# Performance work log

Hardware: AMD Instinct MI355X
Metric: run time of the kernel (lower is better)

## Reference

```python
import jax, jax.numpy as jnp
import numpy as np

DIM_Z = 32      # latent Kalman state dim
DIM_Y = 16      # pseudo-observation dim
K_CLUST = 64    # number of switching clusters
T = 128         # sequence_length
BATCH = 256     # batch_size
INIT_COV = 20.0
NOISE_Q = 0.08  # noise_transition
NOISE_R = 0.03  # noise_emission
INIT_KF = 0.05  # init_kf_matrices (C init scale)


def setup_inputs() -> dict:
    key = jax.random.key(0)
    k1, k2, k3, k4, k5 = jax.random.split(key, 5)
    y = jax.random.normal(k1, (BATCH, T, DIM_Y), jnp.float32)
    dist = jax.random.normal(k2, (BATCH, T, K_CLUST), jnp.float32)
    # A initialized as identity per cluster (plus tiny perturbation so grads are non-trivial)
    A = jnp.broadcast_to(jnp.eye(DIM_Z, dtype=jnp.float32), (K_CLUST, DIM_Z, DIM_Z)) \
        + 0.01 * jax.random.normal(k3, (K_CLUST, DIM_Z, DIM_Z), jnp.float32)
    Bm = 0.01 * jax.random.normal(k4, (K_CLUST, DIM_Z), jnp.float32)  # bias (zeros-init in original)
    C = INIT_KF * jax.random.normal(k5, (K_CLUST, DIM_Y, DIM_Z), jnp.float32)
    return {"y": y, "dist": dist, "A": A, "Bm": Bm, "C": C}


def reference(y, dist, A, Bm, C):
    Q = NOISE_Q * jnp.eye(DIM_Z, dtype=y.dtype)
    R = NOISE_R * jnp.eye(DIM_Y, dtype=y.dtype)
    I = jnp.eye(DIM_Z, dtype=y.dtype)

    mu0 = jnp.zeros((BATCH, DIM_Z), y.dtype)
    Sigma0 = INIT_COV * jnp.broadcast_to(jnp.eye(DIM_Z, dtype=y.dtype), (BATCH, DIM_Z, DIM_Z))
    # first time instant: alpha from dist at t=0 (alphaDistProb ~ softmax over clusters)
    alpha0 = jax.nn.softmax(dist[:, 0, :], axis=-1)

    ys_t = jnp.swapaxes(y, 0, 1)      # [T, B, dim_y]
    dist_t = jnp.swapaxes(dist, 0, 1)  # [T, B, K]

    def step(carry, xs):
        mu_pred, Sigma_pred, alpha = carry
        yt, dt = xs
        # --- update: alpha-mixed emission matrix ---
        C_t = jnp.einsum('bk,kyz->byz', alpha, C)                     # [B, y, z]
        innov = yt - jnp.einsum('byz,bz->by', C_t, mu_pred)
        S = jnp.einsum('byz,bzw,bxw->byx', C_t, Sigma_pred, C_t) + R  # [B, y, y]
        S_inv = jnp.linalg.inv(S)
        K_g = jnp.einsum('bzw,byw,byx->bzx', Sigma_pred, C_t, S_inv)  # Kalman gain [B, z, y]
        mu_f = mu_pred + jnp.einsum('bzy,by->bz', K_g, innov)
        I_KC = I - jnp.einsum('bzy,byw->bzw', K_g, C_t)
        Sigma_f = jnp.einsum('bij,bjk->bik', I_KC, Sigma_pred)
        # --- alpha update (update_alpha_CG_KVAE: combine cluster evidence with prev alpha) ---
        p = jax.nn.softmax(dt, axis=-1) * alpha
        alpha_new = p / jnp.sum(p, axis=-1, keepdims=True)
        # --- predict: alpha-mixed transition ---
        A_t = jnp.einsum('bk,kij->bij', alpha_new, A)
        B_t = alpha_new @ Bm
        mu_pred_new = jnp.einsum('bij,bj->bi', A_t, mu_f) + B_t
        Sigma_pred_new = jnp.einsum('bij,bjk,blk->bil', A_t, Sigma_f, A_t) + Q
        outs = (mu_pred, Sigma_pred, mu_f, Sigma_f, alpha_new, A_t, B_t, C_t)
        return (mu_pred_new, Sigma_pred_new, alpha_new), outs

    _, stacked = jax.lax.scan(step, (mu0, Sigma0, alpha0), (ys_t, dist_t))
    # (mu_preds, Sigma_preds, mu_filts, Sigma_filts, alphas, As, Bs, Cs), each time-major [T, B, ...]
    return stacked
```

## Files before the change

kernel.cpp:

```cpp
#include <hip/hip_runtime.h>
#include <math.h>

#define TT 128
#define BB 256
#define KC 64
#define DZ 32
#define DY 16

#define OFF_MUP   ((size_t)0)
#define OFF_SIGP  (OFF_MUP  + (size_t)TT*BB*DZ)
#define OFF_MUF   (OFF_SIGP + (size_t)TT*BB*DZ*DZ)
#define OFF_SIGF  (OFF_MUF  + (size_t)TT*BB*DZ)
#define OFF_ALPHA (OFF_SIGF + (size_t)TT*BB*DZ*DZ)
#define OFF_AS    (OFF_ALPHA+ (size_t)TT*BB*KC)
#define OFF_BS    (OFF_AS   + (size_t)TT*BB*DZ*DZ)
#define OFF_CS    (OFF_BS   + (size_t)TT*BB*DZ)

#define BAR() do { asm volatile("s_waitcnt lgkmcnt(0)" ::: "memory"); \
                   __builtin_amdgcn_s_barrier(); \
                   asm volatile("" ::: "memory"); } while (0)

__device__ __forceinline__ float wave_max64(float v) {
#pragma unroll
  for (int o = 32; o > 0; o >>= 1) v = fmaxf(v, __shfl_xor(v, o, 64));
  return v;
}
__device__ __forceinline__ float wave_sum64(float v) {
#pragma unroll
  for (int o = 32; o > 0; o >>= 1) v += __shfl_xor(v, o, 64);
  return v;
}
__device__ __forceinline__ float4 shfl4(const float4& v, int src) {
  return make_float4(__shfl(v.x, src, 64), __shfl(v.y, src, 64),
                     __shfl(v.z, src, 64), __shfl(v.w, src, 64));
}
__device__ __forceinline__ float f4get(const float4& v, int e) {
  return e == 0 ? v.x : (e == 1 ? v.y : (e == 2 ? v.z : v.w));
}

__global__ __launch_bounds__(256) void alpha_kernel(const float* __restrict__ dist,
                                                    float* __restrict__ alphas,
                                                    float* __restrict__ beta0) {
  const int b = blockIdx.x;
  const int w = threadIdx.x >> 6;
  const int lane = threadIdx.x & 63;
  const float* db = dist + (size_t)b * TT * KC;

  __shared__ float ls[TT][KC];
  __shared__ float chT[4][KC];
  __shared__ float l0[KC];

  float csum = 0.f;
  for (int tt = 0; tt < 32; ++tt) {
    int t = w * 32 + tt;
    float d = db[t * KC + lane];
    float m = wave_max64(d);
    float e = expf(d - m);
    float s = wave_sum64(e);
    float lsv = d - m - logf(s);
    ls[t][lane] = lsv;
    csum += lsv;
    if (t == 0) l0[lane] = lsv;
  }
  chT[w][lane] = csum;
  __syncthreads();

  float off = l0[lane];
  for (int w2 = 0; w2 < w; ++w2) off += chT[w2][lane];
  if (threadIdx.x < 64) beta0[b * KC + lane] = expf(l0[lane]);

  float run = off;
  for (int tt = 0; tt < 32; ++tt) {
    int t = w * 32 + tt;
    run += ls[t][lane];
    float m = wave_max64(run);
    float e = expf(run - m);
    float s = wave_sum64(e);
    alphas[((size_t)t * BB + b) * KC + lane] = e / s;
  }
}

__global__ __launch_bounds__(256) void mix_kernel(const float* __restrict__ A,
                                                  const float* __restrict__ Bm,
                                                  const float* __restrict__ C,
                                                  const float* __restrict__ alphas,
                                                  const float* __restrict__ beta0,
                                                  float* __restrict__ As,
                                                  float* __restrict__ Bs,
                                                  float* __restrict__ Cs) {
  const int g   = blockIdx.x;
  const int t   = g >> 3;
  const int b0  = (g & 7) << 5;
  const int tid = threadIdx.x;
  const float* arow = alphas + ((size_t)t * BB + b0) * KC;
  const float* brow = (t > 0) ? (alphas + ((size_t)(t - 1) * BB + b0) * KC)
                              : (beta0 + (size_t)b0 * KC);
  const size_t rbase = (size_t)t * BB + b0;

  __shared__ float aS[32][KC];
  __shared__ float bS[32][KC];
  ((float4*)aS)[tid]       = ((const float4*)arow)[tid];
  ((float4*)aS)[tid + 256] = ((const float4*)arow)[tid + 256];
  ((float4*)bS)[tid]       = ((const float4*)brow)[tid];
  ((float4*)bS)[tid + 256] = ((const float4*)brow)[tid + 256];
  __syncthreads();

  {
    const float4* wp = (const float4*)A;
    for (int ch = 0; ch < 2; ++ch) {
      float4 acc[16];
#pragma unroll
      for (int r = 0; r < 16; ++r) acc[r] = make_float4(0.f, 0.f, 0.f, 0.f);
      for (int kk = 0; kk < KC; ++kk) {
        float4 wv = wp[kk * 256 + tid];
#pragma unroll
        for (int r = 0; r < 16; ++r) {
          float a = aS[ch * 16 + r][kk];
          acc[r].x += a * wv.x; acc[r].y += a * wv.y;
          acc[r].z += a * wv.z; acc[r].w += a * wv.w;
        }
      }
#pragma unroll
      for (int r = 0; r < 16; ++r)
        ((float4*)(As + (rbase + ch * 16 + r) * (DZ * DZ)))[tid] = acc[r];
    }
  }
  if (tid < 128) {
    const float4* wp = (const float4*)C;
    for (int ch = 0; ch < 2; ++ch) {
      float4 acc[16];
#pragma unroll
      for (int r = 0; r < 16; ++r) acc[r] = make_float4(0.f, 0.f, 0.f, 0.f);
      for (int kk = 0; kk < KC; ++kk) {
        float4 wv = wp[kk * 128 + tid];
#pragma unroll
        for (int r = 0; r < 16; ++r) {
          float a = bS[ch * 16 + r][kk];
          acc[r].x += a * wv.x; acc[r].y += a * wv.y;
          acc[r].z += a * wv.z; acc[r].w += a * wv.w;
        }
      }
#pragma unroll
      for (int r = 0; r < 16; ++r)
        ((float4*)(Cs + (rbase + ch * 16 + r) * (DY * DZ)))[tid] = acc[r];
    }
  } else if (tid < 192) {
    const int c = (tid - 128) & 7;
    const float4* wp = (const float4*)Bm;
    for (int ch = 0; ch < 2; ++ch) {
      float4 acc[16];
#pragma unroll
      for (int r = 0; r < 16; ++r) acc[r] = make_float4(0.f, 0.f, 0.f, 0.f);
      for (int kk = 0; kk < KC; ++kk) {
        float4 wv = wp[kk * 8 + c];
#pragma unroll
        for (int r = 0; r < 16; ++r) {
          float a = aS[ch * 16 + r][kk];
          acc[r].x += a * wv.x; acc[r].y += a * wv.y;
          acc[r].z += a * wv.z; acc[r].w += a * wv.w;
        }
      }
#pragma unroll
      for (int r = 0; r < 16; ++r)
        ((float4*)(Bs + (rbase + ch * 16 + r) * DZ))[c] = acc[r];
    }
  }
}

__global__ __launch_bounds__(256) void kf_kernel(const float* __restrict__ yin,
                                                 const float* __restrict__ As,
                                                 const float* __restrict__ Bs,
                                                 const float* __restrict__ Cs,
                                                 float* __restrict__ out) {
  const int b   = blockIdx.x;
  const int tid = threadIdx.x;

  __shared__ float Sig[DZ][36];
  __shared__ float Sf [DZ][36];
  __shared__ float Mm [DZ][36];
  __shared__ float At [DZ][36];
  __shared__ float AtT[DZ][36];
  __shared__ float CtT[DZ][24];
  __shared__ float PCt[DZ][24];
  __shared__ float PCtT[DY][36];
  __shared__ float KgT[DY][36];
  __shared__ __align__(16) float mu[DZ];
  __shared__ __align__(16) float muf[DZ];
  __shared__ __align__(16) float Bt[DZ];
  __shared__ float innov[DY], ytl[DY];

  const int i  = tid >> 3;
  const int j0 = (tid & 7) * 4;

#pragma unroll
  for (int q = 0; q < 4; ++q) Sig[i][j0 + q] = (i == j0 + q) ? 20.0f : 0.0f;
  if (tid < DZ) mu[tid] = 0.0f;

  float4 pA, pC = make_float4(0.f, 0.f, 0.f, 0.f);
  float  pB = 0.f, pY = 0.f;
  {
    const size_t tb0 = (size_t)b;
    pA = *(const float4*)(As + tb0 * (DZ * DZ) + tid * 4);
    if (tid < 128)      pC = *(const float4*)(Cs + tb0 * (DY * DZ) + tid * 4);
    else if (tid < 160) pB = Bs[tb0 * DZ + (tid - 128)];
    else if (tid < 176) pY = yin[(size_t)b * TT * DY + (tid - 160)];
  }

  for (int t = 0; t < TT; ++t) {
    const size_t tb = (size_t)t * BB + b;

    *(float4*)&At[i][j0] = pA;
    AtT[j0 + 0][i] = pA.x; AtT[j0 + 1][i] = pA.y;
    AtT[j0 + 2][i] = pA.z; AtT[j0 + 3][i] = pA.w;
    if (tid < 128) {
      int yy = tid >> 3;
      CtT[j0 + 0][yy] = pC.x; CtT[j0 + 1][yy] = pC.y;
      CtT[j0 + 2][yy] = pC.z; CtT[j0 + 3][yy] = pC.w;
    } else if (tid < 160) Bt[tid - 128] = pB;
    else if (tid < 176)   ytl[tid - 160] = pY;

    {
      float4 s4 = *(float4*)&Sig[i][j0];
      *(float4*)(out + OFF_SIGP + tb * (DZ * DZ) + tid * 4) = s4;
      if (tid < DZ) out[OFF_MUP + tb * DZ + tid] = mu[tid];
    }
    {
      int tn = (t + 1 < TT) ? (t + 1) : t;
      size_t tbn = (size_t)tn * BB + b;
      pA = *(const float4*)(As + tbn * (DZ * DZ) + tid * 4);
      if (tid < 128)      pC = *(const float4*)(Cs + tbn * (DY * DZ) + tid * 4);
      else if (tid < 160) pB = Bs[tbn * DZ + (tid - 128)];
      else if (tid < 176) pY = yin[((size_t)b * TT + tn) * DY + (tid - 160)];
    }
    BAR();

    {
      const int z = tid >> 3, xg = (tid >> 1) & 3, h = tid & 1;
      const int x0 = xg * 4, kb = h * 16;
      float4 acc = make_float4(0.f, 0.f, 0.f, 0.f);
#pragma unroll
      for (int k2 = 0; k2 < 16; ++k2) {
        float s = Sig[z][kb + k2];
        float4 c = *(float4*)&CtT[kb + k2][x0];
        acc.x += s * c.x; acc.y += s * c.y; acc.z += s * c.z; acc.w += s * c.w;
      }
      acc.x += __shfl_xor(acc.x, 1, 64); acc.y += __shfl_xor(acc.y, 1, 64);
      acc.z += __shfl_xor(acc.z, 1, 64); acc.w += __shfl_xor(acc.w, 1, 64);
      if (h == 0) {
        *(float4*)&PCt[z][x0] = acc;
        PCtT[x0 + 0][z] = acc.x; PCtT[x0 + 1][z] = acc.y;
        PCtT[x0 + 2][z] = acc.z; PCtT[x0 + 3][z] = acc.w;
      }
    }
    BAR();

    if (tid < 64) {
      const int q = tid >> 2, cg = tid & 3, x0 = cg * 4, base = tid & ~3;
      float4 w0 = make_float4(0.f, 0.f, 0.f, 0.f);
#pragma unroll 8
      for (int z = 0; z < DZ; ++z) {
        float cv = CtT[z][q];
        float4 pv = *(float4*)&PCt[z][x0];
        w0.x += cv * pv.x; w0.y += cv * pv.y; w0.z += cv * pv.z; w0.w += cv * pv.w;
      }
      w0.x += (q == x0 + 0) ? 0.03f : 0.f;
      w0.y += (q == x0 + 1) ? 0.03f : 0.f;
      w0.z += (q == x0 + 2) ? 0.03f : 0.f;
      w0.w += (q == x0 + 3) ? 0.03f : 0.f;
      float4 w1 = *(float4*)&PCtT[q][x0];
      float4 w2 = *(float4*)&PCtT[q][x0 + 16];
#pragma unroll
      for (int p = 0; p < 16; ++p) {
        float4 pr0 = shfl4(w0, 4 * p + cg);
        float4 pr1 = shfl4(w1, 4 * p + cg);
        float4 pr2 = shfl4(w2, 4 * p + cg);
        float pp  = __shfl(f4get(w0, p & 3), 4 * p + (p >> 2), 64);
        float wqp = __shfl(f4get(w0, p & 3), base + (p >> 2), 64);
        float m = (q == p) ? 0.f : (wqp * (1.0f / pp));
        w0.x -= m * pr0.x; w0.y -= m * pr0.y; w0.z -= m * pr0.z; w0.w -= m * pr0.w;
        w1.x -= m * pr1.x; w1.y -= m * pr1.y; w1.z -= m * pr1.z; w1.w -= m * pr1.w;
        w2.x -= m * pr2.x; w2.y -= m * pr2.y; w2.z -= m * pr2.z; w2.w -= m * pr2.w;
      }
      float4 dblk = shfl4(w0, base + (q >> 2));
      float dq = f4get(dblk, q & 3);
      float di = 1.0f / dq;
      *(float4*)&KgT[q][x0]      = make_float4(w1.x * di, w1.y * di, w1.z * di, w1.w * di);
      *(float4*)&KgT[q][x0 + 16] = make_float4(w2.x * di, w2.y * di, w2.z * di, w2.w * di);
    } else if (tid < 128) {
      const int l = tid - 64, yy = l >> 2, zc = (l & 3) * 8;
      float a = 0.f;
#pragma unroll
      for (int r = 0; r < 8; ++r) a += CtT[zc + r][yy] * mu[zc + r];
      a += __shfl_xor(a, 1, 64);
      a += __shfl_xor(a, 2, 64);
      if ((l & 3) == 0) innov[yy] = ytl[yy] - a;
    }
    BAR();

    {
      float4 acc = *(float4*)&Sig[i][j0];
#pragma unroll
      for (int yy = 0; yy < DY; ++yy) {
        float kg = KgT[yy][i];
        float4 pv = *(float4*)&PCtT[yy][j0];
        acc.x -= kg * pv.x; acc.y -= kg * pv.y; acc.z -= kg * pv.z; acc.w -= kg * pv.w;
      }
      *(float4*)&Sf[i][j0] = acc;
      *(float4*)(out + OFF_SIGF + tb * (DZ * DZ) + tid * 4) = acc;
      if (j0 < 16) {
        float s = 0.f;
#pragma unroll
        for (int r = 0; r < 4; ++r) s += KgT[j0 + r][i] * innov[j0 + r];
        s += __shfl_xor(s, 1, 64);
        s += __shfl_xor(s, 2, 64);
        if ((tid & 3) == 0) muf[i] = mu[i] + s;
      }
    }
    BAR();

    {
      float4 acc = make_float4(0.f, 0.f, 0.f, 0.f);
#pragma unroll 8
      for (int k = 0; k < DZ; ++k) {
        float av = At[i][k];
        float4 sv = *(float4*)&Sf[k][j0];
        acc.x += av * sv.x; acc.y += av * sv.y; acc.z += av * sv.z; acc.w += av * sv.w;
      }
      *(float4*)&Mm[i][j0] = acc;
      if (tid < DZ) out[OFF_MUF + tb * DZ + tid] = muf[tid];
    }
    BAR();

    {
      float4 acc = make_float4(0.f, 0.f, 0.f, 0.f);
#pragma unroll 8
      for (int k = 0; k < DZ; ++k) {
        float mv = Mm[i][k];
        float4 av = *(float4*)&AtT[k][j0];
        acc.x += mv * av.x; acc.y += mv * av.y; acc.z += mv * av.z; acc.w += mv * av.w;
      }
      acc.x += (i == j0 + 0) ? 0.08f : 0.f;
      acc.y += (i == j0 + 1) ? 0.08f : 0.f;
      acc.z += (i == j0 + 2) ? 0.08f : 0.f;
      acc.w += (i == j0 + 3) ? 0.08f : 0.f;
      *(float4*)&Sig[i][j0] = acc;

      float4 a4 = *(float4*)&At[i][j0];
      float4 m4 = *(float4*)&muf[j0];
      float s = a4.x * m4.x + a4.y * m4.y + a4.z * m4.z + a4.w * m4.w;
      s += __shfl_xor(s, 1, 64);
      s += __shfl_xor(s, 2, 64);
      s += __shfl_xor(s, 4, 64);
      if ((tid & 7) == 0) mu[i] = Bt[i] + s;
    }
    BAR();
  }
}

extern "C" void kernel_launch(void* const* d_in, const int* in_sizes, int n_in,
                              void* d_out, int out_size, void* d_ws, size_t ws_size,
                              hipStream_t stream) {
  const float* y    = (const float*)d_in[0];
  const float* dist = (const float*)d_in[1];
  const float* A    = (const float*)d_in[2];
  const float* Bm   = (const float*)d_in[3];
  const float* C    = (const float*)d_in[4];
  float* out   = (float*)d_out;
  float* beta0 = (float*)d_ws;

  hipLaunchKernelGGL(alpha_kernel, dim3(BB), dim3(256), 0, stream,
                     dist, out + OFF_ALPHA, beta0);
  hipLaunchKernelGGL(mix_kernel, dim3(TT * BB / 32), dim3(256), 0, stream,
                     A, Bm, C, out + OFF_ALPHA, beta0,
                     out + OFF_AS, out + OFF_BS, out + OFF_CS);
  hipLaunchKernelGGL(kf_kernel, dim3(BB), dim3(256), 0, stream,
                     y, out + OFF_AS, out + OFF_BS, out + OFF_CS, out);
}
```

Measured before the change: 1.295 ms.

## Restructure Kalman step onto bf16x3 MFMA with warp specialization and double buffering

Rewrites the per-step Kalman filter so the matrix products (Sigma·C^T, C·PC^T, A·Sigma·A^T, and the Joseph-like correction terms) run on MFMA using a three-way bf16 split that emulates fp32 accuracy. The covariance prediction is algebraically refactored as A·Sigma·A^T − (A·PC^T)(A·Kg)^T, so the step needs fewer barriers. The four waves are specialized: compute waves, an output and innovation wave, and a prefetch wave that double-buffers A, C, B and y two steps ahead. The mix kernel is also lightly vectorized. The six-MFMA emulation adds instruction overhead and may shift numerics slightly, while most waves sit idle in some phases.

```diff
diff --git a/kernel.cpp b/kernel.cpp
--- a/kernel.cpp
+++ b/kernel.cpp
@@ -16,6 +16,9 @@
 #define OFF_BS    (OFF_AS   + (size_t)TT*BB*DZ*DZ)
 #define OFF_CS    (OFF_BS   + (size_t)TT*BB*DZ)
 
+typedef __attribute__((ext_vector_type(4))) float f4;
+typedef __attribute__((ext_vector_type(8))) short bf16x8;
+
 #define BAR() do { asm volatile("s_waitcnt lgkmcnt(0)" ::: "memory"); \
                    __builtin_amdgcn_s_barrier(); \
                    asm volatile("" ::: "memory"); } while (0)
@@ -30,12 +33,67 @@
   for (int o = 32; o > 0; o >>= 1) v += __shfl_xor(v, o, 64);
   return v;
 }
-__device__ __forceinline__ float4 shfl4(const float4& v, int src) {
-  return make_float4(__shfl(v.x, src, 64), __shfl(v.y, src, 64),
-                     __shfl(v.z, src, 64), __shfl(v.w, src, 64));
-}
-__device__ __forceinline__ float f4get(const float4& v, int e) {
+__device__ __forceinline__ f4 shfl4(f4 v, int src) {
+  f4 r;
+  r.x = __shfl(v.x, src, 64); r.y = __shfl(v.y, src, 64);
+  r.z = __shfl(v.z, src, 64); r.w = __shfl(v.w, src, 64);
+  return r;
+}
+__device__ __forceinline__ float f4get(f4 v, int e) {
   return e == 0 ? v.x : (e == 1 ? v.y : (e == 2 ? v.z : v.w));
+}
+__device__ __forceinline__ float dot4(f4 a, f4 b) {
+  return a.x*b.x + a.y*b.y + a.z*b.z + a.w*b.w;
+}
+
+struct Frag3 { bf16x8 hi; bf16x8 mid; bf16x8 lo; };
+
+__device__ __forceinline__ short bf16rn(float x) {
+  unsigned u = __float_as_uint(x);
+  unsigned r = u + 0x7FFFu + ((u >> 16) & 1u);
+  return (short)(r >> 16);
+}
+__device__ __forceinline__ float bf2f(short s) {
+  return __uint_as_float(((unsigned)(unsigned short)s) << 16);
+}
+__device__ __forceinline__ Frag3 split8(f4 a, f4 b) {
+  Frag3 f;
+  float v[8] = {a.x,a.y,a.z,a.w,b.x,b.y,b.z,b.w};
+#pragma unroll
+  for (int i = 0; i < 8; ++i) {
+    float r = v[i];
+    short h = bf16rn(r);  r -= bf2f(h);
+    short m = bf16rn(r);  r -= bf2f(m);
+    short l = bf16rn(r);
+    f.hi[i] = h; f.mid[i] = m; f.lo[i] = l;
+  }
+  return f;
+}
+__device__ __forceinline__ Frag3 load_frag(const float* base, int ld, int roff, int l) {
+  const float* p = base + ((l & 15) + roff) * ld + (l >> 4) * 8;
+  return split8(*(const f4*)p, *(const f4*)(p + 4));
+}
+__device__ __forceinline__ Frag3 load_frag16(const float* base, int ld, int roff, int l, float sgn) {
+  Frag3 f;
+  if (l < 32) {
+    const float* p = base + ((l & 15) + roff) * ld + (l >> 4) * 8;
+    f4 a = *(const f4*)p * sgn;
+    f4 b = *(const f4*)(p + 4) * sgn;
+    f = split8(a, b);
+  } else {
+    bf16x8 z = {0,0,0,0,0,0,0,0};
+    f.hi = z; f.mid = z; f.lo = z;
+  }
+  return f;
+}
+__device__ __forceinline__ f4 mfma6(const Frag3& A, const Frag3& B, f4 acc) {
+  acc = __builtin_amdgcn_mfma_f32_16x16x32_bf16(A.hi,  B.lo,  acc, 0, 0, 0);
+  acc = __builtin_amdgcn_mfma_f32_16x16x32_bf16(A.mid, B.mid, acc, 0, 0, 0);
+  acc = __builtin_amdgcn_mfma_f32_16x16x32_bf16(A.lo,  B.hi,  acc, 0, 0, 0);
+  acc = __builtin_amdgcn_mfma_f32_16x16x32_bf16(A.hi,  B.mid, acc, 0, 0, 0);
+  acc = __builtin_amdgcn_mfma_f32_16x16x32_bf16(A.mid, B.hi,  acc, 0, 0, 0);
+  acc = __builtin_amdgcn_mfma_f32_16x16x32_bf16(A.hi,  B.hi,  acc, 0, 0, 0);
+  return acc;
 }
 
 __global__ __launch_bounds__(256) void alpha_kernel(const float* __restrict__ dist,
@@ -97,261 +155,309 @@
                               : (beta0 + (size_t)b0 * KC);
   const size_t rbase = (size_t)t * BB + b0;
 
-  __shared__ float aS[32][KC];
-  __shared__ float bS[32][KC];
-  ((float4*)aS)[tid]       = ((const float4*)arow)[tid];
-  ((float4*)aS)[tid + 256] = ((const float4*)arow)[tid + 256];
-  ((float4*)bS)[tid]       = ((const float4*)brow)[tid];
-  ((float4*)bS)[tid + 256] = ((const float4*)brow)[tid + 256];
+  __shared__ __align__(16) float aS[32][KC];
+  __shared__ __align__(16) float bS[32][KC];
+  ((f4*)aS)[tid]       = ((const f4*)arow)[tid];
+  ((f4*)aS)[tid + 256] = ((const f4*)arow)[tid + 256];
+  ((f4*)bS)[tid]       = ((const f4*)brow)[tid];
+  ((f4*)bS)[tid + 256] = ((const f4*)brow)[tid + 256];
   __syncthreads();
 
   {
-    const float4* wp = (const float4*)A;
+    const f4* wp = (const f4*)A;
     for (int ch = 0; ch < 2; ++ch) {
-      float4 acc[16];
-#pragma unroll
-      for (int r = 0; r < 16; ++r) acc[r] = make_float4(0.f, 0.f, 0.f, 0.f);
-      for (int kk = 0; kk < KC; ++kk) {
-        float4 wv = wp[kk * 256 + tid];
+      f4 acc[16];
+#pragma unroll
+      for (int r = 0; r < 16; ++r) acc[r] = (f4){0.f,0.f,0.f,0.f};
+      for (int k4 = 0; k4 < 16; ++k4) {
+        f4 w0 = wp[(k4*4+0)*256 + tid];
+        f4 w1 = wp[(k4*4+1)*256 + tid];
+        f4 w2 = wp[(k4*4+2)*256 + tid];
+        f4 w3 = wp[(k4*4+3)*256 + tid];
 #pragma unroll
         for (int r = 0; r < 16; ++r) {
-          float a = aS[ch * 16 + r][kk];
-          acc[r].x += a * wv.x; acc[r].y += a * wv.y;
-          acc[r].z += a * wv.z; acc[r].w += a * wv.w;
+          f4 a4 = *(const f4*)&aS[ch*16 + r][k4*4];
+          acc[r] += a4.x*w0 + a4.y*w1 + a4.z*w2 + a4.w*w3;
         }
       }
 #pragma unroll
       for (int r = 0; r < 16; ++r)
-        ((float4*)(As + (rbase + ch * 16 + r) * (DZ * DZ)))[tid] = acc[r];
+        ((f4*)(As + (rbase + ch*16 + r) * (DZ*DZ)))[tid] = acc[r];
     }
   }
   if (tid < 128) {
-    const float4* wp = (const float4*)C;
+    const f4* wp = (const f4*)C;
     for (int ch = 0; ch < 2; ++ch) {
-      float4 acc[16];
-#pragma unroll
-      for (int r = 0; r < 16; ++r) acc[r] = make_float4(0.f, 0.f, 0.f, 0.f);
-      for (int kk = 0; kk < KC; ++kk) {
-        float4 wv = wp[kk * 128 + tid];
+      f4 acc[16];
+#pragma unroll
+      for (int r = 0; r < 16; ++r) acc[r] = (f4){0.f,0.f,0.f,0.f};
+      for (int k4 = 0; k4 < 16; ++k4) {
+        f4 w0 = wp[(k4*4+0)*128 + tid];
+        f4 w1 = wp[(k4*4+1)*128 + tid];
+        f4 w2 = wp[(k4*4+2)*128 + tid];
+        f4 w3 = wp[(k4*4+3)*128 + tid];
 #pragma unroll
         for (int r = 0; r < 16; ++r) {
-          float a = bS[ch * 16 + r][kk];
-          acc[r].x += a * wv.x; acc[r].y += a * wv.y;
-          acc[r].z += a * wv.z; acc[r].w += a * wv.w;
+          f4 a4 = *(const f4*)&bS[ch*16 + r][k4*4];
+          acc[r] += a4.x*w0 + a4.y*w1 + a4.z*w2 + a4.w*w3;
         }
       }
 #pragma unroll
       for (int r = 0; r < 16; ++r)
-        ((float4*)(Cs + (rbase + ch * 16 + r) * (DY * DZ)))[tid] = acc[r];
+        ((f4*)(Cs + (rbase + ch*16 + r) * (DY*DZ)))[tid] = acc[r];
     }
   } else if (tid < 192) {
     const int c = (tid - 128) & 7;
-    const float4* wp = (const float4*)Bm;
+    const f4* wb = (const f4*)Bm;
     for (int ch = 0; ch < 2; ++ch) {
-      float4 acc[16];
-#pragma unroll
-      for (int r = 0; r < 16; ++r) acc[r] = make_float4(0.f, 0.f, 0.f, 0.f);
-      for (int kk = 0; kk < KC; ++kk) {
-        float4 wv = wp[kk * 8 + c];
+      f4 acc[16];
+#pragma unroll
+      for (int r = 0; r < 16; ++r) acc[r] = (f4){0.f,0.f,0.f,0.f};
+      for (int k4 = 0; k4 < 16; ++k4) {
+        f4 w0 = wb[(k4*4+0)*8 + c];
+        f4 w1 = wb[(k4*4+1)*8 + c];
+        f4 w2 = wb[(k4*4+2)*8 + c];
+        f4 w3 = wb[(k4*4+3)*8 + c];
 #pragma unroll
         for (int r = 0; r < 16; ++r) {
-          float a = aS[ch * 16 + r][kk];
-          acc[r].x += a * wv.x; acc[r].y += a * wv.y;
-          acc[r].z += a * wv.z; acc[r].w += a * wv.w;
+          f4 a4 = *(const f4*)&aS[ch*16 + r][k4*4];
+          acc[r] += a4.x*w0 + a4.y*w1 + a4.z*w2 + a4.w*w3;
         }
       }
 #pragma unroll
       for (int r = 0; r < 16; ++r)
-        ((float4*)(Bs + (rbase + ch * 16 + r) * DZ))[c] = acc[r];
-    }
-  }
-}
-
-__global__ __launch_bounds__(256) void kf_kernel(const float* __restrict__ yin,
-                                                 const float* __restrict__ As,
-                                                 const float* __restrict__ Bs,
-                                                 const float* __restrict__ Cs,
-                                                 float* __restrict__ out) {
+        ((f4*)(Bs + (rbase + ch*16 + r) * DZ))[c] = acc[r];
+    }
+  }
+}
+
+__global__ __launch_bounds__(256, 1) void kf_kernel(const float* __restrict__ yin,
+                                                    const float* __restrict__ As,
+                                                    const float* __restrict__ Bs,
+                                                    const float* __restrict__ Cs,
+                                                    float* __restrict__ out) {
   const int b   = blockIdx.x;
   const int tid = threadIdx.x;
-
-  __shared__ float Sig[DZ][36];
-  __shared__ float Sf [DZ][36];
-  __shared__ float Mm [DZ][36];
-  __shared__ float At [DZ][36];
-  __shared__ float AtT[DZ][36];
-  __shared__ float CtT[DZ][24];
-  __shared__ float PCt[DZ][24];
-  __shared__ float PCtT[DY][36];
-  __shared__ float KgT[DY][36];
+  const int w   = tid >> 6, l = tid & 63;
+
+  __shared__ __align__(16) float Sig[2][DZ][36];
+  __shared__ __align__(16) float Af [2][DZ][36];
+  __shared__ __align__(16) float Cmx[2][DY][36];
+  __shared__ __align__(16) float Btl[2][DZ];
+  __shared__ __align__(16) float Ytl[2][DY];
+  __shared__ __align__(16) float HT [DZ][36];
+  __shared__ __align__(16) float PClds[DZ][20];
+  __shared__ __align__(16) float PCtT[DY][36];
+  __shared__ __align__(16) float Slds[DY][20];
+  __shared__ __align__(16) float KgT[DY][36];
+  __shared__ __align__(16) float Kglds[DZ][20];
+  __shared__ __align__(16) float APClds[DZ][20];
+  __shared__ __align__(16) float AKlds[DZ][20];
   __shared__ __align__(16) float mu[DZ];
-  __shared__ __align__(16) float muf[DZ];
-  __shared__ __align__(16) float Bt[DZ];
-  __shared__ float innov[DY], ytl[DY];
-
-  const int i  = tid >> 3;
-  const int j0 = (tid & 7) * 4;
-
-#pragma unroll
-  for (int q = 0; q < 4; ++q) Sig[i][j0 + q] = (i == j0 + q) ? 20.0f : 0.0f;
-  if (tid < DZ) mu[tid] = 0.0f;
-
-  float4 pA, pC = make_float4(0.f, 0.f, 0.f, 0.f);
-  float  pB = 0.f, pY = 0.f;
+  __shared__ __align__(16) float mufs[DZ];
+  __shared__ __align__(16) float innov[DY];
+
+  const f4 z4 = {0.f, 0.f, 0.f, 0.f};
+
   {
-    const size_t tb0 = (size_t)b;
-    pA = *(const float4*)(As + tb0 * (DZ * DZ) + tid * 4);
-    if (tid < 128)      pC = *(const float4*)(Cs + tb0 * (DY * DZ) + tid * 4);
-    else if (tid < 160) pB = Bs[tb0 * DZ + (tid - 128)];
-    else if (tid < 176) pY = yin[(size_t)b * TT * DY + (tid - 160)];
-  }
+    size_t t0 = (size_t)b;
+    { int e = tid * 4; *(f4*)&Af[0][e >> 5][e & 31] = *(const f4*)(As + t0 * 1024 + e); }
+    if (tid < 128) { int e = tid * 4; *(f4*)&Cmx[0][e >> 5][e & 31] = *(const f4*)(Cs + t0 * 512 + e); }
+    if (tid < 8)  *(f4*)&Btl[0][tid * 4] = *(const f4*)(Bs + t0 * 32 + tid * 4);
+    if (tid < 4)  *(f4*)&Ytl[0][tid * 4] = *(const f4*)(yin + (size_t)b * TT * DY + tid * 4);
+    int i = tid >> 3, j0 = (tid & 7) * 4;
+#pragma unroll
+    for (int q = 0; q < 4; ++q) Sig[0][i][j0 + q] = (i == j0 + q) ? 20.0f : 0.0f;
+    if (tid < DZ) mu[tid] = 0.f;
+  }
+  f4 pA0, pA1, pA2, pA3, pC0, pC1, pBv, pYv;
+  if (w == 3) {
+    size_t t1 = (size_t)1 * BB + b;
+    pA0 = *(const f4*)(As + t1*1024 + (0*64 + l)*4);
+    pA1 = *(const f4*)(As + t1*1024 + (1*64 + l)*4);
+    pA2 = *(const f4*)(As + t1*1024 + (2*64 + l)*4);
+    pA3 = *(const f4*)(As + t1*1024 + (3*64 + l)*4);
+    pC0 = *(const f4*)(Cs + t1*512 + (0*64 + l)*4);
+    pC1 = *(const f4*)(Cs + t1*512 + (1*64 + l)*4);
+    if (l < 8)              pBv = *(const f4*)(Bs + t1*32 + l*4);
+    else if (l < 12)        pYv = *(const f4*)(yin + ((size_t)b*TT + 1)*DY + (l-8)*4);
+  }
+  __syncthreads();
 
   for (int t = 0; t < TT; ++t) {
+    const int cur = t & 1, nxt = cur ^ 1;
     const size_t tb = (size_t)t * BB + b;
-
-    *(float4*)&At[i][j0] = pA;
-    AtT[j0 + 0][i] = pA.x; AtT[j0 + 1][i] = pA.y;
-    AtT[j0 + 2][i] = pA.z; AtT[j0 + 3][i] = pA.w;
-    if (tid < 128) {
-      int yy = tid >> 3;
-      CtT[j0 + 0][yy] = pC.x; CtT[j0 + 1][yy] = pC.y;
-      CtT[j0 + 2][yy] = pC.z; CtT[j0 + 3][yy] = pC.w;
-    } else if (tid < 160) Bt[tid - 128] = pB;
-    else if (tid < 176)   ytl[tid - 160] = pY;
-
-    {
-      float4 s4 = *(float4*)&Sig[i][j0];
-      *(float4*)(out + OFF_SIGP + tb * (DZ * DZ) + tid * 4) = s4;
-      if (tid < DZ) out[OFF_MUP + tb * DZ + tid] = mu[tid];
-    }
-    {
-      int tn = (t + 1 < TT) ? (t + 1) : t;
-      size_t tbn = (size_t)tn * BB + b;
-      pA = *(const float4*)(As + tbn * (DZ * DZ) + tid * 4);
-      if (tid < 128)      pC = *(const float4*)(Cs + tbn * (DY * DZ) + tid * 4);
-      else if (tid < 160) pB = Bs[tbn * DZ + (tid - 128)];
-      else if (tid < 176) pY = yin[((size_t)b * TT + tn) * DY + (tid - 160)];
+    const int c = l & 15, rg = l >> 4;
+
+    Frag3 f_cB, f_aB0, f_aB1;
+    f4 g00 = z4, g01 = z4, g10 = z4, g11 = z4;
+
+    if (w == 0) {
+      Frag3 sA0 = load_frag(&Sig[cur][0][0], 36, 0,  l);
+      Frag3 sA1 = load_frag(&Sig[cur][0][0], 36, 16, l);
+      f_cB      = load_frag(&Cmx[cur][0][0], 36, 0,  l);
+      f4 pc0 = mfma6(sA0, f_cB, z4);
+      f4 pc1 = mfma6(sA1, f_cB, z4);
+#pragma unroll
+      for (int m = 0; m < 4; ++m) {
+        PClds[rg*4 + m][c]      = f4get(pc0, m);
+        PClds[16 + rg*4 + m][c] = f4get(pc1, m);
+      }
+      *(f4*)&PCtT[c][rg*4]      = pc0;
+      *(f4*)&PCtT[c][16 + rg*4] = pc1;
+    } else if (w == 1) {
+      Frag3 gA0 = load_frag(&Sig[cur][0][0], 36, 0,  l);
+      Frag3 gA1 = load_frag(&Sig[cur][0][0], 36, 16, l);
+      f_aB0 = load_frag(&Af[cur][0][0], 36, 0,  l);
+      f_aB1 = load_frag(&Af[cur][0][0], 36, 16, l);
+      f4 h00 = mfma6(gA0, f_aB0, z4);
+      f4 h01 = mfma6(gA0, f_aB1, z4);
+      f4 h10 = mfma6(gA1, f_aB0, z4);
+      f4 h11 = mfma6(gA1, f_aB1, z4);
+      *(f4*)&HT[c][rg*4]           = h00;
+      *(f4*)&HT[16 + c][rg*4]      = h01;
+      *(f4*)&HT[c][16 + rg*4]      = h10;
+      *(f4*)&HT[16 + c][16 + rg*4] = h11;
+      Frag3 hA0 = load_frag(&HT[0][0], 36, 0,  l);
+      Frag3 hA1 = load_frag(&HT[0][0], 36, 16, l);
+      g00 = mfma6(hA0, f_aB0, z4);  g01 = mfma6(hA0, f_aB1, z4);
+      g10 = mfma6(hA1, f_aB0, z4);  g11 = mfma6(hA1, f_aB1, z4);
+    } else if (w == 2) {
+      int yy = l >> 2, p = l & 3, k0 = p * 8;
+      f4 c0 = *(const f4*)&Cmx[cur][yy][k0], c1 = *(const f4*)&Cmx[cur][yy][k0 + 4];
+      f4 m0 = *(const f4*)&mu[k0],           m1 = *(const f4*)&mu[k0 + 4];
+      float a = dot4(c0, m0) + dot4(c1, m1);
+      a += __shfl_xor(a, 1, 64);
+      a += __shfl_xor(a, 2, 64);
+      if (p == 0) innov[yy] = Ytl[cur][yy] - a;
+#pragma unroll
+      for (int m = 0; m < 4; ++m) {
+        int e = (m*64 + l) * 4;
+        f4 v = *(const f4*)&Sig[cur][e >> 5][e & 31];
+        *(f4*)(out + OFF_SIGP + tb * 1024 + e) = v;
+      }
+      if (l < DZ) out[OFF_MUP + tb * DZ + l] = mu[l];
+    } else {
+      { int e = (0*64 + l)*4; *(f4*)&Af[nxt][e >> 5][e & 31] = pA0; }
+      { int e = (1*64 + l)*4; *(f4*)&Af[nxt][e >> 5][e & 31] = pA1; }
+      { int e = (2*64 + l)*4; *(f4*)&Af[nxt][e >> 5][e & 31] = pA2; }
+      { int e = (3*64 + l)*4; *(f4*)&Af[nxt][e >> 5][e & 31] = pA3; }
+      { int e = (0*64 + l)*4; *(f4*)&Cmx[nxt][e >> 5][e & 31] = pC0; }
+      { int e = (1*64 + l)*4; *(f4*)&Cmx[nxt][e >> 5][e & 31] = pC1; }
+      if (l < 8)       *(f4*)&Btl[nxt][l*4] = pBv;
+      else if (l < 12) *(f4*)&Ytl[nxt][(l-8)*4] = pYv;
+      int tf = (t + 2 < TT) ? (t + 2) : (TT - 1);
+      size_t tbf = (size_t)tf * BB + b;
+      pA0 = *(const f4*)(As + tbf*1024 + (0*64 + l)*4);
+      pA1 = *(const f4*)(As + tbf*1024 + (1*64 + l)*4);
+      pA2 = *(const f4*)(As + tbf*1024 + (2*64 + l)*4);
+      pA3 = *(const f4*)(As + tbf*1024 + (3*64 + l)*4);
+      pC0 = *(const f4*)(Cs + tbf*512 + (0*64 + l)*4);
+      pC1 = *(const f4*)(Cs + tbf*512 + (1*64 + l)*4);
+      if (l < 8)       pBv = *(const f4*)(Bs + tbf*32 + l*4);
+      else if (l < 12) pYv = *(const f4*)(yin + ((size_t)b*TT + tf)*DY + (l-8)*4);
     }
     BAR();
 
-    {
-      const int z = tid >> 3, xg = (tid >> 1) & 3, h = tid & 1;
-      const int x0 = xg * 4, kb = h * 16;
-      float4 acc = make_float4(0.f, 0.f, 0.f, 0.f);
-#pragma unroll
-      for (int k2 = 0; k2 < 16; ++k2) {
-        float s = Sig[z][kb + k2];
-        float4 c = *(float4*)&CtT[kb + k2][x0];
-        acc.x += s * c.x; acc.y += s * c.y; acc.z += s * c.z; acc.w += s * c.w;
-      }
-      acc.x += __shfl_xor(acc.x, 1, 64); acc.y += __shfl_xor(acc.y, 1, 64);
-      acc.z += __shfl_xor(acc.z, 1, 64); acc.w += __shfl_xor(acc.w, 1, 64);
-      if (h == 0) {
-        *(float4*)&PCt[z][x0] = acc;
-        PCtT[x0 + 0][z] = acc.x; PCtT[x0 + 1][z] = acc.y;
-        PCtT[x0 + 2][z] = acc.z; PCtT[x0 + 3][z] = acc.w;
-      }
-    }
-    BAR();
-
-    if (tid < 64) {
-      const int q = tid >> 2, cg = tid & 3, x0 = cg * 4, base = tid & ~3;
-      float4 w0 = make_float4(0.f, 0.f, 0.f, 0.f);
-#pragma unroll 8
-      for (int z = 0; z < DZ; ++z) {
-        float cv = CtT[z][q];
-        float4 pv = *(float4*)&PCt[z][x0];
-        w0.x += cv * pv.x; w0.y += cv * pv.y; w0.z += cv * pv.z; w0.w += cv * pv.w;
-      }
-      w0.x += (q == x0 + 0) ? 0.03f : 0.f;
-      w0.y += (q == x0 + 1) ? 0.03f : 0.f;
-      w0.z += (q == x0 + 2) ? 0.03f : 0.f;
-      w0.w += (q == x0 + 3) ? 0.03f : 0.f;
-      float4 w1 = *(float4*)&PCtT[q][x0];
-      float4 w2 = *(float4*)&PCtT[q][x0 + 16];
+    if (w == 0) {
+      Frag3 pB = load_frag(&PCtT[0][0], 36, 0, l);
+      f4 s = mfma6(f_cB, pB, z4);
+#pragma unroll
+      for (int m = 0; m < 4; ++m)
+        Slds[rg*4 + m][c] = f4get(s, m) + ((rg*4 + m) == c ? 0.03f : 0.f);
+      const int q = l >> 2, cg = l & 3, base = l & ~3;
+      f4 w0 = *(const f4*)&Slds[q][cg*4];
+      f4 w1 = *(const f4*)&PCtT[q][cg*4];
+      f4 w2 = *(const f4*)&PCtT[q][16 + cg*4];
 #pragma unroll
       for (int p = 0; p < 16; ++p) {
-        float4 pr0 = shfl4(w0, 4 * p + cg);
-        float4 pr1 = shfl4(w1, 4 * p + cg);
-        float4 pr2 = shfl4(w2, 4 * p + cg);
-        float pp  = __shfl(f4get(w0, p & 3), 4 * p + (p >> 2), 64);
+        f4 pr0 = shfl4(w0, 4*p + cg);
+        f4 pr1 = shfl4(w1, 4*p + cg);
+        f4 pr2 = shfl4(w2, 4*p + cg);
+        float pp  = __shfl(f4get(w0, p & 3), 4*p + (p >> 2), 64);
         float wqp = __shfl(f4get(w0, p & 3), base + (p >> 2), 64);
         float m = (q == p) ? 0.f : (wqp * (1.0f / pp));
-        w0.x -= m * pr0.x; w0.y -= m * pr0.y; w0.z -= m * pr0.z; w0.w -= m * pr0.w;
-        w1.x -= m * pr1.x; w1.y -= m * pr1.y; w1.z -= m * pr1.z; w1.w -= m * pr1.w;
-        w2.x -= m * pr2.x; w2.y -= m * pr2.y; w2.z -= m * pr2.z; w2.w -= m * pr2.w;
-      }
-      float4 dblk = shfl4(w0, base + (q >> 2));
-      float dq = f4get(dblk, q & 3);
-      float di = 1.0f / dq;
-      *(float4*)&KgT[q][x0]      = make_float4(w1.x * di, w1.y * di, w1.z * di, w1.w * di);
-      *(float4*)&KgT[q][x0 + 16] = make_float4(w2.x * di, w2.y * di, w2.z * di, w2.w * di);
-    } else if (tid < 128) {
-      const int l = tid - 64, yy = l >> 2, zc = (l & 3) * 8;
-      float a = 0.f;
-#pragma unroll
-      for (int r = 0; r < 8; ++r) a += CtT[zc + r][yy] * mu[zc + r];
-      a += __shfl_xor(a, 1, 64);
-      a += __shfl_xor(a, 2, 64);
-      if ((l & 3) == 0) innov[yy] = ytl[yy] - a;
+        w0 -= m * pr0; w1 -= m * pr1; w2 -= m * pr2;
+      }
+      f4 dblk = shfl4(w0, base + (q >> 2));
+      float di = 1.0f / f4get(dblk, q & 3);
+      f4 w1d = w1 * di, w2d = w2 * di;
+      *(f4*)&KgT[q][cg*4]      = w1d;
+      *(f4*)&KgT[q][16 + cg*4] = w2d;
+#pragma unroll
+      for (int e = 0; e < 4; ++e) {
+        Kglds[cg*4 + e][q]      = f4get(w1d, e);
+        Kglds[16 + cg*4 + e][q] = f4get(w2d, e);
+      }
+    } else if (w == 2) {
+      Frag3 aA0 = load_frag(&Af[cur][0][0], 36, 0,  l);
+      Frag3 aA1 = load_frag(&Af[cur][0][0], 36, 16, l);
+      Frag3 pcB = load_frag(&PCtT[0][0], 36, 0, l);
+      f4 ap0 = mfma6(aA0, pcB, z4);
+      f4 ap1 = mfma6(aA1, pcB, z4);
+#pragma unroll
+      for (int m = 0; m < 4; ++m) {
+        APClds[rg*4 + m][c]      = f4get(ap0, m);
+        APClds[16 + rg*4 + m][c] = f4get(ap1, m);
+      }
     }
     BAR();
 
-    {
-      float4 acc = *(float4*)&Sig[i][j0];
-#pragma unroll
-      for (int yy = 0; yy < DY; ++yy) {
-        float kg = KgT[yy][i];
-        float4 pv = *(float4*)&PCtT[yy][j0];
-        acc.x -= kg * pv.x; acc.y -= kg * pv.y; acc.z -= kg * pv.z; acc.w -= kg * pv.w;
-      }
-      *(float4*)&Sf[i][j0] = acc;
-      *(float4*)(out + OFF_SIGF + tb * (DZ * DZ) + tid * 4) = acc;
-      if (j0 < 16) {
-        float s = 0.f;
-#pragma unroll
-        for (int r = 0; r < 4; ++r) s += KgT[j0 + r][i] * innov[j0 + r];
-        s += __shfl_xor(s, 1, 64);
-        s += __shfl_xor(s, 2, 64);
-        if ((tid & 3) == 0) muf[i] = mu[i] + s;
-      }
-    }
-    BAR();
-
-    {
-      float4 acc = make_float4(0.f, 0.f, 0.f, 0.f);
-#pragma unroll 8
-      for (int k = 0; k < DZ; ++k) {
-        float av = At[i][k];
-        float4 sv = *(float4*)&Sf[k][j0];
-        acc.x += av * sv.x; acc.y += av * sv.y; acc.z += av * sv.z; acc.w += av * sv.w;
-      }
-      *(float4*)&Mm[i][j0] = acc;
-      if (tid < DZ) out[OFF_MUF + tb * DZ + tid] = muf[tid];
-    }
-    BAR();
-
-    {
-      float4 acc = make_float4(0.f, 0.f, 0.f, 0.f);
-#pragma unroll 8
-      for (int k = 0; k < DZ; ++k) {
-        float mv = Mm[i][k];
-        float4 av = *(float4*)&AtT[k][j0];
-        acc.x += mv * av.x; acc.y += mv * av.y; acc.z += mv * av.z; acc.w += mv * av.w;
-      }
-      acc.x += (i == j0 + 0) ? 0.08f : 0.f;
-      acc.y += (i == j0 + 1) ? 0.08f : 0.f;
-      acc.z += (i == j0 + 2) ? 0.08f : 0.f;
-      acc.w += (i == j0 + 3) ? 0.08f : 0.f;
-      *(float4*)&Sig[i][j0] = acc;
-
-      float4 a4 = *(float4*)&At[i][j0];
-      float4 m4 = *(float4*)&muf[j0];
-      float s = a4.x * m4.x + a4.y * m4.y + a4.z * m4.z + a4.w * m4.w;
+    if (w == 0) {
+      if (l < DZ) {
+        float a = mu[l];
+#pragma unroll
+        for (int y = 0; y < DY; ++y) a += KgT[y][l] * innov[y];
+        mufs[l] = a;
+        out[OFF_MUF + tb * DZ + l] = a;
+      }
+      int i = l >> 1, h = l & 1, k0 = h * 16;
+      f4 a0 = *(const f4*)&Af[cur][i][k0],     a1 = *(const f4*)&Af[cur][i][k0 + 4];
+      f4 a2 = *(const f4*)&Af[cur][i][k0 + 8], a3 = *(const f4*)&Af[cur][i][k0 + 12];
+      f4 m0 = *(const f4*)&mufs[k0],     m1 = *(const f4*)&mufs[k0 + 4];
+      f4 m2 = *(const f4*)&mufs[k0 + 8], m3 = *(const f4*)&mufs[k0 + 12];
+      float s = dot4(a0,m0) + dot4(a1,m1) + dot4(a2,m2) + dot4(a3,m3);
       s += __shfl_xor(s, 1, 64);
-      s += __shfl_xor(s, 2, 64);
-      s += __shfl_xor(s, 4, 64);
-      if ((tid & 7) == 0) mu[i] = Bt[i] + s;
+      if (h == 0) mu[i] = s + Btl[cur][i];
+    } else if (w == 1) {
+      Frag3 kB = load_frag(&KgT[0][0], 36, 0, l);
+      f4 ak0 = mfma6(f_aB0, kB, z4);
+      f4 ak1 = mfma6(f_aB1, kB, z4);
+#pragma unroll
+      for (int m = 0; m < 4; ++m) {
+        AKlds[rg*4 + m][c]      = f4get(ak0, m);
+        AKlds[16 + rg*4 + m][c] = f4get(ak1, m);
+      }
+      Frag3 apA0 = load_frag16(&APClds[0][0], 20, 0,  l,  1.f);
+      Frag3 apA1 = load_frag16(&APClds[0][0], 20, 16, l,  1.f);
+      Frag3 akB0 = load_frag16(&AKlds[0][0],  20, 0,  l, -1.f);
+      Frag3 akB1 = load_frag16(&AKlds[0][0],  20, 16, l, -1.f);
+      g00 = mfma6(apA0, akB0, g00);  g01 = mfma6(apA0, akB1, g01);
+      g10 = mfma6(apA1, akB0, g10);  g11 = mfma6(apA1, akB1, g11);
+#pragma unroll
+      for (int m = 0; m < 4; ++m) {
+        if (rg*4 + m == c) { g00[m] += 0.08f; g11[m] += 0.08f; }
+      }
+      *(f4*)&Sig[nxt][c][rg*4]           = g00;
+      *(f4*)&Sig[nxt][16 + c][rg*4]      = g01;
+      *(f4*)&Sig[nxt][c][16 + rg*4]      = g10;
+      *(f4*)&Sig[nxt][16 + c][16 + rg*4] = g11;
+    } else if (w == 2) {
+      Frag3 pA0  = load_frag16(&PClds[0][0], 20, 0,  l,  1.f);
+      Frag3 pA1  = load_frag16(&PClds[0][0], 20, 16, l,  1.f);
+      Frag3 kgB0 = load_frag16(&Kglds[0][0], 20, 0,  l, -1.f);
+      Frag3 kgB1 = load_frag16(&Kglds[0][0], 20, 16, l, -1.f);
+      f4 sf00 = *(const f4*)&Sig[cur][c][rg*4];
+      f4 sf01 = *(const f4*)&Sig[cur][16 + c][rg*4];
+      f4 sf10 = *(const f4*)&Sig[cur][c][16 + rg*4];
+      f4 sf11 = *(const f4*)&Sig[cur][16 + c][16 + rg*4];
+      sf00 = mfma6(pA0, kgB0, sf00);  sf01 = mfma6(pA0, kgB1, sf01);
+      sf10 = mfma6(pA1, kgB0, sf10);  sf11 = mfma6(pA1, kgB1, sf11);
+      float* o = out + OFF_SIGF + tb * 1024;
+      *(f4*)(o + (c)*32 + rg*4)             = sf00;
+      *(f4*)(o + (16 + c)*32 + rg*4)        = sf01;
+      *(f4*)(o + (c)*32 + 16 + rg*4)        = sf10;
+      *(f4*)(o + (16 + c)*32 + 16 + rg*4)   = sf11;
     }
     BAR();
   }
```

Result: faster. 1.260 ms (-2.7%).
